# Optimization experiments

Hardware: AMD Instinct MI355X
Metric: run time of the kernel (lower is better)

## Reference

```python
import jax, jax.numpy as jnp
import numpy as np

B, T, F, E, H, D, L = 4096, 20, 32, 128, 2, 64, 3
EPS = 1e-5


def setup_inputs() -> dict:
    key = jax.random.key(0)
    ks = jax.random.split(key, 16)
    n = lambda k, s, sc=0.05: jax.random.normal(k, s, jnp.float32) * sc
    return {
        'tokens': jax.random.randint(ks[0], (B, T), 0, 50000),
        'field_ids': jax.random.randint(ks[1], (B, F - 1), 0, 1000),
        'word_emb': n(ks[2], (50000, 300)),
        'W_tok': n(ks[3], (300, E)),
        'field_tables': n(ks[4], (F - 1, 1000, E), E ** -0.5),
        'Wq': n(ks[5], (L, E, H * D)),
        'Wk': n(ks[6], (L, E, H * D)),
        'Wv': n(ks[7], (L, E, H * D)),
        'Wres': n(ks[8], (L, E, H * D)),
        'ln_g': jnp.ones((L, H * D), jnp.float32),
        'ln_b': jnp.zeros((L, H * D), jnp.float32),
        'dnn_W1': n(ks[9], (F * E, 1024)),
        'bn1_g': jnp.ones((1024,), jnp.float32), 'bn1_b': jnp.zeros((1024,), jnp.float32),
        'bn1_m': jnp.zeros((1024,), jnp.float32), 'bn1_v': jnp.ones((1024,), jnp.float32),
        'dnn_W2': n(ks[10], (1024, 512)),
        'bn2_g': jnp.ones((512,), jnp.float32), 'bn2_b': jnp.zeros((512,), jnp.float32),
        'bn2_m': jnp.zeros((512,), jnp.float32), 'bn2_v': jnp.ones((512,), jnp.float32),
        'dnn_W3': n(ks[11], (512, 128)),
        'dnn_b3': jnp.zeros((128,), jnp.float32),
        'W_last': n(ks[12], (F * H * D + 128, 1)),
        'b_last': jnp.zeros((1,), jnp.float32),
    }


def _layer_norm(o, g, b):
    mu = o.mean(-1, keepdims=True)
    var = o.var(-1, keepdims=True)
    return (o - mu) / jnp.sqrt(var + EPS) * g + b


def reference(tokens, field_ids, word_emb, W_tok, field_tables, Wq, Wk, Wv, Wres,
              ln_g, ln_b, dnn_W1, bn1_g, bn1_b, bn1_m, bn1_v, dnn_W2, bn2_g, bn2_b,
              bn2_m, bn2_v, dnn_W3, dnn_b3, W_last, b_last):
    # EmbeddingBag(mean) over tokens, then linear to emb_length
    tok_e = word_emb[tokens].mean(1) @ W_tok                      # [B, E]
    # per-field one-hot embedding lookup
    fld_e = field_tables[jnp.arange(F - 1)[None, :], field_ids]    # [B, F-1, E]
    emb = jnp.concatenate([tok_e[:, None, :], fld_e], 1)          # [B, F, E]

    x = emb
    for l in range(L):
        # split(num_out,-1)+cat(...,0) == reshape to heads
        q = (x @ Wq[l]).reshape(B, F, H, D)
        k = (x @ Wk[l]).reshape(B, F, H, D)
        v = (x @ Wv[l]).reshape(B, F, H, D)
        w = jax.nn.softmax(jnp.einsum('bqhd,bkhd->bhqk', q, k) / jnp.sqrt(jnp.float32(D)), -1)
        o = jnp.einsum('bhqk,bkhd->bqhd', w, v).reshape(B, F, H * D)
        o = jax.nn.relu(o + x @ Wres[l])
        x = _layer_norm(o, ln_g[l], ln_b[l])

    att = x.reshape(B, F * H * D)

    # DNN branch (eval mode: BN uses running stats, dropout off)
    h = emb.reshape(B, F * E)
    h = jax.nn.relu((h @ dnn_W1 - bn1_m) / jnp.sqrt(bn1_v + EPS) * bn1_g + bn1_b)
    h = jax.nn.relu((h @ dnn_W2 - bn2_m) / jnp.sqrt(bn2_v + EPS) * bn2_g + bn2_b)
    h = h @ dnn_W3 + dnn_b3

    out = jnp.concatenate([att, h], 1) @ W_last + b_last          # [B, 1]
    return jax.nn.sigmoid(out)
```

## Files before the change

kernel.cpp:

```cpp
#include <hip/hip_runtime.h>
#include <hip/hip_bf16.h>
#include <cstdint>

#define B_  4096
#define T_  20
#define F_  32
#define E_  128
#define H_  2
#define D_  64
#define L_  3
#define HD_ 128
#define EPS_ 1e-5f

typedef __bf16 bfv8 __attribute__((ext_vector_type(8)));
typedef __bf16 bfv4 __attribute__((ext_vector_type(4)));
typedef float  f32x4 __attribute__((ext_vector_type(4)));

__device__ __forceinline__ f32x4 mfma16(bfv8 a, bfv8 b, f32x4 c) {
    return __builtin_amdgcn_mfma_f32_16x16x32_bf16(a, b, c, 0, 0, 0);
}

__device__ __forceinline__ void gload16(const __bf16* g, __bf16* l) {
    __builtin_amdgcn_global_load_lds(
        (const __attribute__((address_space(1))) void*)(g),
        (__attribute__((address_space(3))) void*)(l),
        16, 0, 0);
}

__global__ __launch_bounds__(256) void pack_weights_kernel(
    const float* __restrict__ Wq, const float* __restrict__ Wk,
    const float* __restrict__ Wv, const float* __restrict__ Wres,
    __bf16* __restrict__ out)
{
    int mi = blockIdx.x;
    int tile = blockIdx.y;
    int l = mi >> 2, p = mi & 3;
    const float* Wb = (p == 0 ? Wq : p == 1 ? Wk : p == 2 ? Wv : Wres) + l * 16384;
    int tid = threadIdx.x;
    int ks = tid >> 6, lane = tid & 63;
    int l15 = lane & 15, lgg = lane >> 4;
    const float* src = Wb + (ks * 32 + lgg * 8) * HD_ + tile * 16 + l15;
    __bf16* dst = out + (int64_t)mi * 16384 + ((tile * 4 + ks) * 64 + lane) * 8;
    #pragma unroll
    for (int t = 0; t < 8; t++) dst[t] = (__bf16)src[t * HD_];
}

__global__ __launch_bounds__(256) void transpose_pack_kernel(
    const float* __restrict__ in, __bf16* __restrict__ out, int K, int N)
{
    __shared__ float t[64][65];
    int k0 = blockIdx.x * 64, n0 = blockIdx.y * 64;
    int r = threadIdx.x >> 4, c = (threadIdx.x & 15) * 4;
    for (int rr = r; rr < 64; rr += 16) {
        float4 v = *(const float4*)&in[(int64_t)(k0 + rr) * N + n0 + c];
        t[rr][c] = v.x; t[rr][c + 1] = v.y; t[rr][c + 2] = v.z; t[rr][c + 3] = v.w;
    }
    __syncthreads();
    for (int rr = r; rr < 64; rr += 16) {
        bfv4 o;
        o[0] = (__bf16)t[c + 0][rr];
        o[1] = (__bf16)t[c + 1][rr];
        o[2] = (__bf16)t[c + 2][rr];
        o[3] = (__bf16)t[c + 3][rr];
        *(bfv4*)&out[(int64_t)(n0 + rr) * K + k0 + c] = o;
    }
}

__global__ __launch_bounds__(128) void tok_embed_kernel(
    const int* __restrict__ tokens, const float* __restrict__ word_emb,
    const float* __restrict__ W_tok, __bf16* __restrict__ embbf)
{
    int b = blockIdx.x;
    int tid = threadIdx.x;
    __shared__ float m[300];
    float a0 = 0.f, a1 = 0.f, a2 = 0.f;
    const int* tb = tokens + b * T_;
    for (int t = 0; t < T_; t++) {
        const float* row = word_emb + (int64_t)tb[t] * 300;
        a0 += row[tid];
        a1 += row[tid + 128];
        if (tid < 44) a2 += row[tid + 256];
    }
    m[tid]       = a0 * (1.f / T_);
    m[tid + 128] = a1 * (1.f / T_);
    if (tid < 44) m[tid + 256] = a2 * (1.f / T_);
    __syncthreads();
    float s = 0.f;
    for (int e = 0; e < 300; e++) s = fmaf(m[e], W_tok[e * E_ + tid], s);
    embbf[(int64_t)b * (F_ * E_) + tid] = (__bf16)s;
}

__global__ __launch_bounds__(256) void field_gather_kernel(
    const int* __restrict__ field_ids, const float* __restrict__ field_tables,
    __bf16* __restrict__ embbf)
{
    int64_t idx = (int64_t)blockIdx.x * blockDim.x + threadIdx.x;
    if (idx >= (int64_t)B_ * 31 * 32) return;
    int c = (int)(idx & 31);
    int64_t tmp = idx >> 5;
    int f = (int)(tmp % 31);
    int b = (int)(tmp / 31);
    int id = field_ids[b * 31 + f];
    const float4* src = (const float4*)field_tables;
    float4 val = src[(int64_t)(f * 1000 + id) * 32 + c];
    bfv4 o;
    o[0] = (__bf16)val.x; o[1] = (__bf16)val.y;
    o[2] = (__bf16)val.z; o[3] = (__bf16)val.w;
    *(bfv4*)&embbf[(int64_t)b * 4096 + (1 + f) * 128 + c * 4] = o;
}

template <int OUTBF, int EPI>
__global__ __launch_bounds__(256) void gemm_bt_bf16(
    const __bf16* __restrict__ A, const __bf16* __restrict__ Bt,
    void* __restrict__ Cout, int M, int N, int K,
    const float* __restrict__ gp, const float* __restrict__ bp,
    const float* __restrict__ mp, const float* __restrict__ vp)
{
    __shared__ __bf16 As[128 * 64];
    __shared__ __bf16 Bs[64 * 64];
    const int tid = threadIdx.x;
    const int wid = tid >> 6, lane = tid & 63;
    const int l15 = lane & 15, lg = lane >> 4;
    const int wr = wid >> 1, wc = wid & 1;
    const int bm = blockIdx.x, bn = blockIdx.y;

    const int srow = lane >> 3, sp = lane & 7;
    const __bf16* Ag[4]; const __bf16* Bg[2];
    __bf16* Ad[4]; __bf16* Bd[2];
    #pragma unroll
    for (int ga = 0; ga < 4; ga++) {
        int row = wid * 32 + ga * 8 + srow;
        int slot = sp ^ (row & 7);
        Ag[ga] = A + (int64_t)(bm * 128 + row) * K + slot * 8;
        Ad[ga] = &As[(wid * 32 + ga * 8) * 64];
    }
    #pragma unroll
    for (int gb = 0; gb < 2; gb++) {
        int row = wid * 16 + gb * 8 + srow;
        int slot = sp ^ (row & 7);
        Bg[gb] = Bt + (int64_t)(bn * 64 + row) * K + slot * 8;
        Bd[gb] = &Bs[(wid * 16 + gb * 8) * 64];
    }

    int ar[2][4], br2[2][2];
    #pragma unroll
    for (int ks = 0; ks < 2; ks++) {
        #pragma unroll
        for (int mi = 0; mi < 4; mi++) {
            int row = wr * 64 + mi * 16 + l15;
            ar[ks][mi] = row * 64 + (((ks * 4 + lg) ^ (row & 7)) * 8);
        }
        #pragma unroll
        for (int ni = 0; ni < 2; ni++) {
            int row = wc * 32 + ni * 16 + l15;
            br2[ks][ni] = row * 64 + (((ks * 4 + lg) ^ (row & 7)) * 8);
        }
    }

    f32x4 acc[4][2];
    #pragma unroll
    for (int mi = 0; mi < 4; mi++)
        #pragma unroll
        for (int ni = 0; ni < 2; ni++) acc[mi][ni] = (f32x4){0.f, 0.f, 0.f, 0.f};

    for (int k0 = 0; k0 < K; k0 += 64) {
        #pragma unroll
        for (int ga = 0; ga < 4; ga++) gload16(Ag[ga] + k0, Ad[ga]);
        #pragma unroll
        for (int gb = 0; gb < 2; gb++) gload16(Bg[gb] + k0, Bd[gb]);
        __syncthreads();
        #pragma unroll
        for (int ks = 0; ks < 2; ks++) {
            bfv8 af[4], bf2[2];
            #pragma unroll
            for (int mi = 0; mi < 4; mi++) af[mi] = *(const bfv8*)&As[ar[ks][mi]];
            #pragma unroll
            for (int ni = 0; ni < 2; ni++) bf2[ni] = *(const bfv8*)&Bs[br2[ks][ni]];
            #pragma unroll
            for (int mi = 0; mi < 4; mi++)
                #pragma unroll
                for (int ni = 0; ni < 2; ni++)
                    acc[mi][ni] = mfma16(af[mi], bf2[ni], acc[mi][ni]);
        }
        __syncthreads();
    }

    float inv[2], sh[2];
    #pragma unroll
    for (int ni = 0; ni < 2; ni++) {
        int col = bn * 64 + wc * 32 + ni * 16 + l15;
        if constexpr (EPI == 0) {
            float iv = rsqrtf(vp[col] + EPS_) * gp[col];
            inv[ni] = iv;
            sh[ni] = bp[col] - mp[col] * iv;
        } else {
            inv[ni] = 1.f;
            sh[ni] = bp[col];
        }
    }
    #pragma unroll
    for (int mi = 0; mi < 4; mi++)
        #pragma unroll
        for (int ni = 0; ni < 2; ni++) {
            int col = bn * 64 + wc * 32 + ni * 16 + l15;
            #pragma unroll
            for (int r = 0; r < 4; r++) {
                int row = bm * 128 + wr * 64 + mi * 16 + lg * 4 + r;
                float y = fmaf(acc[mi][ni][r], inv[ni], sh[ni]);
                if constexpr (EPI == 0) y = fmaxf(y, 0.f);
                if constexpr (OUTBF)
                    ((__bf16*)Cout)[(int64_t)row * N + col] = (__bf16)y;
                else
                    ((float*)Cout)[(int64_t)row * N + col] = y;
            }
        }
}

__global__ __launch_bounds__(512, 4) void attn3_head_kernel(
    const __bf16* __restrict__ embbf, const __bf16* __restrict__ pkw,
    const float* __restrict__ lng, const float* __restrict__ lnb,
    const float* __restrict__ h3, const float* __restrict__ Wl,
    const float* __restrict__ bl, float* __restrict__ out)
{
    __shared__ __bf16 xs[2][32 * 128];
    __shared__ __bf16 q_lds[2][32 * 128];
    __shared__ __bf16 k_lds[2][32 * 128];
    __shared__ __bf16 vt_lds[2][128 * 32];
    __shared__ __bf16 p_lds[8 * 512];
    __shared__ float  part[2][128];

    const int tid = threadIdx.x;
    const int wid = tid >> 6, lane = tid & 63;
    const int l15 = lane & 15, lg = lane >> 4;
    const int arow = wid >> 2, h = (wid >> 1) & 1, qh = wid & 1;
    const int q = qh * 16 + l15;

    {
        const __bf16* src = embbf + (int64_t)blockIdx.x * 8192;
        #pragma unroll
        for (int u = 0; u < 2; u++) {
            int c = tid * 2 + u;
            int brow = c >> 9, fld = (c >> 4) & 31, slot = c & 15;
            bfv8 v = *(const bfv8*)&src[brow * 4096 + fld * 128 + slot * 8];
            *(bfv8*)&xs[brow][fld * 128 + ((slot * 8) ^ ((fld & 7) << 3))] = v;
        }
    }
    __syncthreads();

    float head_partial = 0.f;

    for (int l = 0; l < L_; l++) {
        #pragma unroll 1
        for (int cc = 0; cc < 3; cc++) {
            const int col = wid * 3 + cc;
            const int mat = col >> 3, m = col & 7;
            const __bf16* W = pkw + (l * 4 + mat) * 16384;
            bfv8 wf[4];
            #pragma unroll
            for (int ks = 0; ks < 4; ks++)
                wf[ks] = *(const bfv8*)(W + ((m * 4 + ks) * 64 + lane) * 8);
            f32x4 pc[4];
            #pragma unroll
            for (int i = 0; i < 4; i++) pc[i] = (f32x4){0.f, 0.f, 0.f, 0.f};

            if (mat == 2) {
                #pragma unroll
                for (int i = 0; i < 4; i++) {
                    int br = i >> 1, fld = (i & 1) * 16 + l15;
                    #pragma unroll
                    for (int ks = 0; ks < 4; ks++) {
                        bfv8 xv = *(const bfv8*)&xs[br][fld * 128 + ((ks * 32 + lg * 8) ^ ((fld & 7) << 3))];
                        pc[i] = mfma16(xv, wf[ks], pc[i]);
                    }
                }
            } else {
                #pragma unroll
                for (int i = 0; i < 4; i++) {
                    int br = i >> 1, fld = (i & 1) * 16 + l15;
                    #pragma unroll
                    for (int ks = 0; ks < 4; ks++) {
                        bfv8 xv = *(const bfv8*)&xs[br][fld * 128 + ((ks * 32 + lg * 8) ^ ((fld & 7) << 3))];
                        pc[i] = mfma16(wf[ks], xv, pc[i]);
                    }
                }
            }

            if (mat == 0) {
                #pragma unroll
                for (int i = 0; i < 4; i++) {
                    int br = i >> 1, fld = (i & 1) * 16 + l15;
                    int j = m * 16 + lg * 4;
                    bfv4 v4;
                    #pragma unroll
                    for (int r = 0; r < 4; r++) v4[r] = (__bf16)(pc[i][r] * 0.125f);
                    *(bfv4*)&q_lds[br][fld * 128 + (j ^ ((fld & 7) << 3))] = v4;
                }
            } else if (mat == 1) {
                #pragma unroll
                for (int i = 0; i < 4; i++) {
                    int br = i >> 1, fld = (i & 1) * 16 + l15;
                    int j = m * 16 + lg * 4;
                    bfv4 v4;
                    #pragma unroll
                    for (int r = 0; r < 4; r++) v4[r] = (__bf16)pc[i][r];
                    *(bfv4*)&k_lds[br][fld * 128 + (j ^ ((fld & 7) << 3))] = v4;
                }
            } else {
                #pragma unroll
                for (int i = 0; i < 4; i++) {
                    int br = i >> 1;
                    int d = m * 16 + l15;
                    int key = (i & 1) * 16 + lg * 4;
                    bfv4 v4;
                    #pragma unroll
                    for (int r = 0; r < 4; r++) v4[r] = (__bf16)pc[i][r];
                    *(bfv4*)&vt_lds[br][d * 32 + (key ^ (((d >> 1) & 3) << 3))] = v4;
                }
            }
        }

        f32x4 macc[4];
        {
            const __bf16* Wr = pkw + (l * 4 + 3) * 16384;
            bfv8 xr[4];
            #pragma unroll
            for (int ks = 0; ks < 4; ks++)
                xr[ks] = *(const bfv8*)&xs[arow][q * 128 + ((ks * 32 + lg * 8) ^ ((q & 7) << 3))];
            #pragma unroll
            for (int dm = 0; dm < 4; dm++) {
                macc[dm] = (f32x4){0.f, 0.f, 0.f, 0.f};
                int m = h * 4 + dm;
                #pragma unroll
                for (int ks = 0; ks < 4; ks++) {
                    bfv8 wf = *(const bfv8*)(Wr + ((m * 4 + ks) * 64 + lane) * 8);
                    macc[dm] = mfma16(wf, xr[ks], macc[dm]);
                }
            }
        }
        __syncthreads();

        f32x4 sc2[2] = {(f32x4){0.f, 0.f, 0.f, 0.f}, (f32x4){0.f, 0.f, 0.f, 0.f}};
        #pragma unroll
        for (int ks = 0; ks < 2; ks++) {
            int d = h * 64 + ks * 32 + lg * 8;
            bfv8 qb = *(const bfv8*)&q_lds[arow][q * 128 + (d ^ ((q & 7) << 3))];
            #pragma unroll
            for (int km = 0; km < 2; km++) {
                int key = km * 16 + l15;
                bfv8 kb = *(const bfv8*)&k_lds[arow][key * 128 + (d ^ ((key & 7) << 3))];
                sc2[km] = mfma16(kb, qb, sc2[km]);
            }
        }

        float mx = -1e30f;
        #pragma unroll
        for (int km = 0; km < 2; km++)
            #pragma unroll
            for (int r = 0; r < 4; r++) mx = fmaxf(mx, sc2[km][r]);
        mx = fmaxf(mx, __shfl_xor(mx, 16));
        mx = fmaxf(mx, __shfl_xor(mx, 32));
        float pv[2][4];
        float sum = 0.f;
        #pragma unroll
        for (int km = 0; km < 2; km++)
            #pragma unroll
            for (int r = 0; r < 4; r++) {
                float e = __expf(sc2[km][r] - mx);
                pv[km][r] = e; sum += e;
            }
        sum += __shfl_xor(sum, 16);
        sum += __shfl_xor(sum, 32);
        float inv = 1.f / sum;

        __bf16* pw = p_lds + wid * 512;
        #pragma unroll
        for (int km = 0; km < 2; km++) {
            int key = km * 16 + lg * 4;
            bfv4 v4;
            #pragma unroll
            for (int r = 0; r < 4; r++) v4[r] = (__bf16)(pv[km][r] * inv);
            *(bfv4*)&pw[l15 * 32 + (key ^ (((l15 >> 1) & 3) << 3))] = v4;
        }

        bfv8 pb = *(const bfv8*)&pw[l15 * 32 + ((lg * 8) ^ (((l15 >> 1) & 3) << 3))];
        f32x4 o[4];
        #pragma unroll
        for (int dm = 0; dm < 4; dm++) {
            int d = h * 64 + dm * 16 + l15;
            bfv8 va = *(const bfv8*)&vt_lds[arow][d * 32 + ((lg * 8) ^ (((d >> 1) & 3) << 3))];
            o[dm] = mfma16(va, pb, (f32x4){0.f, 0.f, 0.f, 0.f});
        }

        float yv[4][4];
        float s1 = 0.f, s2 = 0.f;
        #pragma unroll
        for (int dm = 0; dm < 4; dm++) {
            #pragma unroll
            for (int r = 0; r < 4; r++) {
                float v = fmaxf(o[dm][r] + macc[dm][r], 0.f);
                yv[dm][r] = v;
                s1 += v; s2 += v * v;
            }
        }
        s1 += __shfl_xor(s1, 16); s1 += __shfl_xor(s1, 32);
        s2 += __shfl_xor(s2, 16); s2 += __shfl_xor(s2, 32);
        if (lg == 0) { part[arow][q * 4 + h * 2] = s1; part[arow][q * 4 + h * 2 + 1] = s2; }
        __syncthreads();

        f32x4 pt = *(const f32x4*)&part[arow][q * 4];
        float mean = (pt[0] + pt[2]) * (1.f / 128.f);
        float var  = (pt[1] + pt[3]) * (1.f / 128.f) - mean * mean;
        float rstd = rsqrtf(var + EPS_);
        const float* lgp = lng + l * HD_;
        const float* lbp = lnb + l * HD_;

        if (l < L_ - 1) {
            #pragma unroll
            for (int dm = 0; dm < 4; dm++) {
                int j = h * 64 + dm * 16 + lg * 4;
                float4 g  = *(const float4*)(lgp + j);
                float4 bb = *(const float4*)(lbp + j);
                bfv4 y;
                y[0] = (__bf16)((yv[dm][0] - mean) * rstd * g.x + bb.x);
                y[1] = (__bf16)((yv[dm][1] - mean) * rstd * g.y + bb.y);
                y[2] = (__bf16)((yv[dm][2] - mean) * rstd * g.z + bb.z);
                y[3] = (__bf16)((yv[dm][3] - mean) * rstd * g.w + bb.w);
                *(bfv4*)&xs[arow][q * 128 + (j ^ ((q & 7) << 3))] = y;
            }
            __syncthreads();
        } else {
            #pragma unroll
            for (int dm = 0; dm < 4; dm++) {
                int j = h * 64 + dm * 16 + lg * 4;
                float4 g  = *(const float4*)(lgp + j);
                float4 bb = *(const float4*)(lbp + j);
                float4 w  = *(const float4*)(Wl + q * HD_ + j);
                head_partial = fmaf((yv[dm][0] - mean) * rstd * g.x + bb.x, w.x, head_partial);
                head_partial = fmaf((yv[dm][1] - mean) * rstd * g.y + bb.y, w.y, head_partial);
                head_partial = fmaf((yv[dm][2] - mean) * rstd * g.z + bb.z, w.z, head_partial);
                head_partial = fmaf((yv[dm][3] - mean) * rstd * g.w + bb.w, w.w, head_partial);
            }
        }
    }

    float* red = (float*)p_lds;
    red[tid] = head_partial;
    __syncthreads();
    if ((wid & 3) == 0) {
        int br = wid >> 2;
        int base = br * 256;
        float s = red[base + lane] + red[base + 64 + lane]
                + red[base + 128 + lane] + red[base + 192 + lane];
        int64_t b0 = (int64_t)blockIdx.x * 2 + br;
        s += h3[b0 * 128 + lane]      * Wl[4096 + lane];
        s += h3[b0 * 128 + 64 + lane] * Wl[4096 + 64 + lane];
        #pragma unroll
        for (int off = 32; off; off >>= 1) s += __shfl_down(s, off);
        if (lane == 0) out[b0] = 1.f / (1.f + __expf(-(s + bl[0])));
    }
}

extern "C" void kernel_launch(void* const* d_in, const int* in_sizes, int n_in,
                              void* d_out, int out_size, void* d_ws, size_t ws_size,
                              hipStream_t stream)
{
    const int*   tokens       = (const int*)  d_in[0];
    const int*   field_ids    = (const int*)  d_in[1];
    const float* word_emb     = (const float*)d_in[2];
    const float* W_tok        = (const float*)d_in[3];
    const float* field_tables = (const float*)d_in[4];
    const float* Wq           = (const float*)d_in[5];
    const float* Wk           = (const float*)d_in[6];
    const float* Wv           = (const float*)d_in[7];
    const float* Wres         = (const float*)d_in[8];
    const float* ln_g         = (const float*)d_in[9];
    const float* ln_b         = (const float*)d_in[10];
    const float* dnn_W1       = (const float*)d_in[11];
    const float* bn1_g        = (const float*)d_in[12];
    const float* bn1_b        = (const float*)d_in[13];
    const float* bn1_m        = (const float*)d_in[14];
    const float* bn1_v        = (const float*)d_in[15];
    const float* dnn_W2       = (const float*)d_in[16];
    const float* bn2_g        = (const float*)d_in[17];
    const float* bn2_b        = (const float*)d_in[18];
    const float* bn2_m        = (const float*)d_in[19];
    const float* bn2_v        = (const float*)d_in[20];
    const float* dnn_W3       = (const float*)d_in[21];
    const float* dnn_b3       = (const float*)d_in[22];
    const float* W_last       = (const float*)d_in[23];
    const float* b_last       = (const float*)d_in[24];
    float* out = (float*)d_out;

    const int64_t embN = (int64_t)B_ * F_ * E_;
    __bf16* embbf = (__bf16*)d_ws;
    float*  h3    = (float*)(embbf + embN);
    __bf16* pkw   = (__bf16*)(h3 + (int64_t)B_ * 128);
    __bf16* W1t   = pkw + 12 * 16384;
    __bf16* W2t   = W1t + (int64_t)1024 * 4096;
    __bf16* W3t   = W2t + (int64_t)512 * 1024;
    __bf16* h1bf  = W3t + (int64_t)128 * 512;
    __bf16* h2bf  = h1bf + (int64_t)B_ * 1024;

    pack_weights_kernel<<<dim3(12, 8), 256, 0, stream>>>(Wq, Wk, Wv, Wres, pkw);
    transpose_pack_kernel<<<dim3(64, 16), 256, 0, stream>>>(dnn_W1, W1t, 4096, 1024);
    transpose_pack_kernel<<<dim3(16, 8), 256, 0, stream>>>(dnn_W2, W2t, 1024, 512);
    transpose_pack_kernel<<<dim3(8, 2), 256, 0, stream>>>(dnn_W3, W3t, 512, 128);

    tok_embed_kernel<<<B_, 128, 0, stream>>>(tokens, word_emb, W_tok, embbf);
    field_gather_kernel<<<(B_ * 31 * 32) / 256, 256, 0, stream>>>(field_ids, field_tables, embbf);

    gemm_bt_bf16<1, 0><<<dim3(32, 16), 256, 0, stream>>>(
        embbf, W1t, h1bf, B_, 1024, 4096, bn1_g, bn1_b, bn1_m, bn1_v);
    gemm_bt_bf16<1, 0><<<dim3(32, 8), 256, 0, stream>>>(
        h1bf, W2t, h2bf, B_, 512, 1024, bn2_g, bn2_b, bn2_m, bn2_v);
    gemm_bt_bf16<0, 1><<<dim3(32, 2), 256, 0, stream>>>(
        h2bf, W3t, h3, B_, 128, 512, nullptr, dnn_b3, nullptr, nullptr);

    attn3_head_kernel<<<B_ / 2, 512, 0, stream>>>(
        embbf, pkw, ln_g, ln_b, h3, W_last, b_last, out);
}
```

Before: 249.8 us.

## Store attention operands in MFMA-fragment order and stage Wres in LDS

Changes the LDS layout of x, Q, K, V^T and P from XOR-swizzled row-major to pre-packed MFMA fragment order, so each lane reads its operand with one contiguous 16-byte load at lane*8 and no swizzle arithmetic. The residual projection weight Wres is now staged into LDS asynchronously (global_load_lds), reusing the Q buffer after the score computation. The residual matmul moves after the PV product, which adds an extra barrier per layer. The goal is to cut address math and global weight reads from every wave, at the cost of more syncs and a reordered schedule.

```diff
diff --git a/kernel.cpp b/kernel.cpp
--- a/kernel.cpp
+++ b/kernel.cpp
@@ -222,27 +222,33 @@
     const float* __restrict__ h3, const float* __restrict__ Wl,
     const float* __restrict__ bl, float* __restrict__ out)
 {
-    __shared__ __bf16 xs[2][32 * 128];
-    __shared__ __bf16 q_lds[2][32 * 128];
-    __shared__ __bf16 k_lds[2][32 * 128];
-    __shared__ __bf16 vt_lds[2][128 * 32];
-    __shared__ __bf16 p_lds[8 * 512];
+    __shared__ __bf16 smem[8192 * 4 + 4096];
     __shared__ float  part[2][128];
+    __bf16* xs  = smem;
+    __bf16* qf  = smem + 8192;
+    __bf16* kf  = smem + 16384;
+    __bf16* vtf = smem + 24576;
+    __bf16* pf  = smem + 32768;
+    __bf16* wrs = qf;
 
     const int tid = threadIdx.x;
     const int wid = tid >> 6, lane = tid & 63;
     const int l15 = lane & 15, lg = lane >> 4;
     const int arow = wid >> 2, h = (wid >> 1) & 1, qh = wid & 1;
     const int q = qh * 16 + l15;
+    const int half = (lg & 1) * 4;
 
     {
         const __bf16* src = embbf + (int64_t)blockIdx.x * 8192;
         #pragma unroll
         for (int u = 0; u < 2; u++) {
-            int c = tid * 2 + u;
-            int brow = c >> 9, fld = (c >> 4) & 31, slot = c & 15;
-            bfv8 v = *(const bfv8*)&src[brow * 4096 + fld * 128 + slot * 8];
-            *(bfv8*)&xs[brow][fld * 128 + ((slot * 8) ^ ((fld & 7) << 3))] = v;
+            int g = u * 512 + tid;
+            int ln = g & 63;
+            int fld = (((g >> 8) & 1) << 4) + (ln & 15);
+            int e0 = ((g >> 6) & 3) * 32 + (ln >> 4) * 8;
+            int br = g >> 9;
+            bfv8 v = *(const bfv8*)&src[br * 4096 + fld * 128 + e0];
+            *(bfv8*)&xs[g * 8] = v;
         }
     }
     __syncthreads();
@@ -266,92 +272,80 @@
             if (mat == 2) {
                 #pragma unroll
                 for (int i = 0; i < 4; i++) {
-                    int br = i >> 1, fld = (i & 1) * 16 + l15;
+                    int gbase = ((i >> 1) * 8 + (i & 1) * 4) * 64;
                     #pragma unroll
                     for (int ks = 0; ks < 4; ks++) {
-                        bfv8 xv = *(const bfv8*)&xs[br][fld * 128 + ((ks * 32 + lg * 8) ^ ((fld & 7) << 3))];
+                        bfv8 xv = *(const bfv8*)&xs[(gbase + ks * 64 + lane) * 8];
                         pc[i] = mfma16(xv, wf[ks], pc[i]);
                     }
                 }
             } else {
                 #pragma unroll
                 for (int i = 0; i < 4; i++) {
-                    int br = i >> 1, fld = (i & 1) * 16 + l15;
+                    int gbase = ((i >> 1) * 8 + (i & 1) * 4) * 64;
                     #pragma unroll
                     for (int ks = 0; ks < 4; ks++) {
-                        bfv8 xv = *(const bfv8*)&xs[br][fld * 128 + ((ks * 32 + lg * 8) ^ ((fld & 7) << 3))];
+                        bfv8 xv = *(const bfv8*)&xs[(gbase + ks * 64 + lane) * 8];
                         pc[i] = mfma16(wf[ks], xv, pc[i]);
                     }
                 }
             }
 
             if (mat == 0) {
+                const int ln2 = ((((m << 1) + (lg >> 1)) & 3) << 4) + l15;
                 #pragma unroll
                 for (int i = 0; i < 4; i++) {
-                    int br = i >> 1, fld = (i & 1) * 16 + l15;
-                    int j = m * 16 + lg * 4;
                     bfv4 v4;
                     #pragma unroll
                     for (int r = 0; r < 4; r++) v4[r] = (__bf16)(pc[i][r] * 0.125f);
-                    *(bfv4*)&q_lds[br][fld * 128 + (j ^ ((fld & 7) << 3))] = v4;
+                    int g = ((i >> 1) * 8 + (i & 1) * 4 + (m >> 1)) * 64 + ln2;
+                    *(bfv4*)&qf[g * 8 + half] = v4;
                 }
             } else if (mat == 1) {
+                const int ln2 = ((((m << 1) + (lg >> 1)) & 3) << 4) + l15;
                 #pragma unroll
                 for (int i = 0; i < 4; i++) {
-                    int br = i >> 1, fld = (i & 1) * 16 + l15;
-                    int j = m * 16 + lg * 4;
                     bfv4 v4;
                     #pragma unroll
                     for (int r = 0; r < 4; r++) v4[r] = (__bf16)pc[i][r];
-                    *(bfv4*)&k_lds[br][fld * 128 + (j ^ ((fld & 7) << 3))] = v4;
+                    int g = ((i >> 1) * 8 + (i & 1) * 4 + (m >> 1)) * 64 + ln2;
+                    *(bfv4*)&kf[g * 8 + half] = v4;
                 }
             } else {
                 #pragma unroll
                 for (int i = 0; i < 4; i++) {
-                    int br = i >> 1;
-                    int d = m * 16 + l15;
-                    int key = (i & 1) * 16 + lg * 4;
                     bfv4 v4;
                     #pragma unroll
                     for (int r = 0; r < 4; r++) v4[r] = (__bf16)pc[i][r];
-                    *(bfv4*)&vt_lds[br][d * 32 + (key ^ (((d >> 1) & 3) << 3))] = v4;
+                    int lnv = ((((i & 1) * 2 + (lg >> 1)) & 3) << 4) + l15;
+                    int g = ((i >> 1) * 8 + m) * 64 + lnv;
+                    *(bfv4*)&vtf[g * 8 + half] = v4;
                 }
             }
         }
-
-        f32x4 macc[4];
+        __syncthreads();
+
+        f32x4 sc2[2] = {(f32x4){0.f, 0.f, 0.f, 0.f}, (f32x4){0.f, 0.f, 0.f, 0.f}};
+        #pragma unroll
+        for (int ksp = 0; ksp < 2; ksp++) {
+            int dks = h * 2 + ksp;
+            bfv8 qb = *(const bfv8*)&qf[((arow * 8 + qh * 4 + dks) * 64 + lane) * 8];
+            #pragma unroll
+            for (int km = 0; km < 2; km++) {
+                bfv8 kb = *(const bfv8*)&kf[((arow * 8 + km * 4 + dks) * 64 + lane) * 8];
+                sc2[km] = mfma16(kb, qb, sc2[km]);
+            }
+        }
+        __syncthreads();
+
         {
             const __bf16* Wr = pkw + (l * 4 + 3) * 16384;
-            bfv8 xr[4];
-            #pragma unroll
-            for (int ks = 0; ks < 4; ks++)
-                xr[ks] = *(const bfv8*)&xs[arow][q * 128 + ((ks * 32 + lg * 8) ^ ((q & 7) << 3))];
-            #pragma unroll
-            for (int dm = 0; dm < 4; dm++) {
-                macc[dm] = (f32x4){0.f, 0.f, 0.f, 0.f};
-                int m = h * 4 + dm;
-                #pragma unroll
-                for (int ks = 0; ks < 4; ks++) {
-                    bfv8 wf = *(const bfv8*)(Wr + ((m * 4 + ks) * 64 + lane) * 8);
-                    macc[dm] = mfma16(wf, xr[ks], macc[dm]);
-                }
-            }
-        }
-        __syncthreads();
-
-        f32x4 sc2[2] = {(f32x4){0.f, 0.f, 0.f, 0.f}, (f32x4){0.f, 0.f, 0.f, 0.f}};
-        #pragma unroll
-        for (int ks = 0; ks < 2; ks++) {
-            int d = h * 64 + ks * 32 + lg * 8;
-            bfv8 qb = *(const bfv8*)&q_lds[arow][q * 128 + (d ^ ((q & 7) << 3))];
-            #pragma unroll
-            for (int km = 0; km < 2; km++) {
-                int key = km * 16 + l15;
-                bfv8 kb = *(const bfv8*)&k_lds[arow][key * 128 + (d ^ ((key & 7) << 3))];
-                sc2[km] = mfma16(kb, qb, sc2[km]);
-            }
-        }
-
+            #pragma unroll
+            for (int c = 0; c < 4; c++) {
+                int g = c * 512 + tid;
+                gload16(Wr + g * 8, wrs + g * 8);
+            }
+        }
         float mx = -1e30f;
         #pragma unroll
         for (int km = 0; km < 2; km++)
@@ -372,23 +366,40 @@
         sum += __shfl_xor(sum, 32);
         float inv = 1.f / sum;
 
-        __bf16* pw = p_lds + wid * 512;
+        __bf16* pw = pf + wid * 512;
         #pragma unroll
         for (int km = 0; km < 2; km++) {
-            int key = km * 16 + lg * 4;
+            int ln2 = (((km * 2 + (lg >> 1)) & 3) << 4) + l15;
             bfv4 v4;
             #pragma unroll
             for (int r = 0; r < 4; r++) v4[r] = (__bf16)(pv[km][r] * inv);
-            *(bfv4*)&pw[l15 * 32 + (key ^ (((l15 >> 1) & 3) << 3))] = v4;
-        }
-
-        bfv8 pb = *(const bfv8*)&pw[l15 * 32 + ((lg * 8) ^ (((l15 >> 1) & 3) << 3))];
+            *(bfv4*)&pw[ln2 * 8 + half] = v4;
+        }
+        bfv8 pb = *(const bfv8*)&pw[lane * 8];
         f32x4 o[4];
         #pragma unroll
         for (int dm = 0; dm < 4; dm++) {
-            int d = h * 64 + dm * 16 + l15;
-            bfv8 va = *(const bfv8*)&vt_lds[arow][d * 32 + ((lg * 8) ^ (((d >> 1) & 3) << 3))];
+            bfv8 va = *(const bfv8*)&vtf[((arow * 8 + h * 4 + dm) * 64 + lane) * 8];
             o[dm] = mfma16(va, pb, (f32x4){0.f, 0.f, 0.f, 0.f});
+        }
+        __syncthreads();
+
+        f32x4 macc[4];
+        {
+            bfv8 xr[4];
+            #pragma unroll
+            for (int ks = 0; ks < 4; ks++)
+                xr[ks] = *(const bfv8*)&xs[((arow * 8 + qh * 4 + ks) * 64 + lane) * 8];
+            #pragma unroll
+            for (int dm = 0; dm < 4; dm++) {
+                macc[dm] = (f32x4){0.f, 0.f, 0.f, 0.f};
+                int m = h * 4 + dm;
+                #pragma unroll
+                for (int ks = 0; ks < 4; ks++) {
+                    bfv8 wf = *(const bfv8*)&wrs[((m * 4 + ks) * 64 + lane) * 8];
+                    macc[dm] = mfma16(wf, xr[ks], macc[dm]);
+                }
+            }
         }
 
         float yv[4][4];
@@ -425,7 +436,10 @@
                 y[1] = (__bf16)((yv[dm][1] - mean) * rstd * g.y + bb.y);
                 y[2] = (__bf16)((yv[dm][2] - mean) * rstd * g.z + bb.z);
                 y[3] = (__bf16)((yv[dm][3] - mean) * rstd * g.w + bb.w);
-                *(bfv4*)&xs[arow][q * 128 + (j ^ ((q & 7) << 3))] = y;
+                int ks2 = h * 2 + (dm >> 1);
+                int ln2 = (((dm * 2 + (lg >> 1)) & 3) << 4) + l15;
+                int g2 = (arow * 8 + qh * 4 + ks2) * 64 + ln2;
+                *(bfv4*)&xs[g2 * 8 + half] = y;
             }
             __syncthreads();
         } else {
@@ -443,7 +457,7 @@
         }
     }
 
-    float* red = (float*)p_lds;
+    float* red = (float*)pf;
     red[tid] = head_partial;
     __syncthreads();
     if ((wid & 3) == 0) {
```

Result: faster. 237.7 us (-4.8%).
